# Kernel optimization log

Measured on AMD Instinct MI355X. Metric: run time of the kernel, lower is better.

The kernel has to match this reference:

```python
import jax, jax.numpy as jnp
import numpy as np

B = 128          # graphs per batch
NPG = 512        # nodes per graph
N = B * NPG      # 65536 nodes
E = 262144       # edges, avg degree 4, intra-graph only
IN_FEATS = 128
EDGE_FEATS = 32
EMB = 64
HEADS = 4
HC = EMB * HEADS  # 256
L = 3


def setup_inputs():
    ki = iter(jax.random.split(jax.random.key(0), 64))

    def nrm(shape):
        return jax.random.normal(next(ki), shape, jnp.float32)

    def lin(fan_in, shape):
        return jax.random.uniform(next(ki), shape, jnp.float32, -1.0, 1.0) / np.float32(np.sqrt(fan_in))

    x = nrm((N, IN_FEATS))
    edge_attr = nrm((E, EDGE_FEATS))
    g = jnp.arange(E) // (E // B)  # each edge stays inside its graph
    src = g * NPG + jax.random.randint(next(ki), (E,), 0, NPG)
    dst = g * NPG + jax.random.randint(next(ki), (E,), 0, NPG)
    edge_index = jnp.stack([src, dst]).astype(jnp.int32)
    batch_index = (jnp.arange(N) // NPG).astype(jnp.int32)
    d = dict(x=x, edge_attr=edge_attr, edge_index=edge_index, batch_index=batch_index)
    d['Wq1'] = lin(IN_FEATS, (IN_FEATS, HC)); d['bq1'] = lin(IN_FEATS, (HC,))
    d['Wk1'] = lin(IN_FEATS, (IN_FEATS, HC)); d['bk1'] = lin(IN_FEATS, (HC,))
    d['Wv1'] = lin(IN_FEATS, (IN_FEATS, HC)); d['bv1'] = lin(IN_FEATS, (HC,))
    d['We1'] = lin(EDGE_FEATS, (EDGE_FEATS, HC))
    d['Wskip1'] = lin(IN_FEATS, (IN_FEATS, HC)); d['bskip1'] = lin(IN_FEATS, (HC,))
    d['Wbeta1'] = lin(3 * HC, (3 * HC,))
    d['Wt1'] = lin(HC, (HC, EMB)); d['bt1'] = lin(HC, (EMB,))
    d['bng1'] = jnp.ones((EMB,), jnp.float32); d['bnb1'] = jnp.zeros((EMB,), jnp.float32)
    d['Wq'] = lin(EMB, (L, EMB, HC)); d['bq'] = lin(EMB, (L, HC))
    d['Wk'] = lin(EMB, (L, EMB, HC)); d['bk'] = lin(EMB, (L, HC))
    d['Wv'] = lin(EMB, (L, EMB, HC)); d['bv'] = lin(EMB, (L, HC))
    d['We'] = lin(EDGE_FEATS, (L, EDGE_FEATS, HC))
    d['Wskip'] = lin(EMB, (L, EMB, HC)); d['bskip'] = lin(EMB, (L, HC))
    d['Wbeta'] = lin(3 * HC, (L, 3 * HC))
    d['Wt'] = lin(HC, (L, HC, EMB)); d['bt'] = lin(HC, (L, EMB))
    d['bng'] = jnp.ones((L, EMB), jnp.float32); d['bnb'] = jnp.zeros((L, EMB), jnp.float32)
    d['pw0'] = lin(EMB, (EMB,)); d['pw2'] = lin(EMB, (EMB,))
    return d


def _tconv(x, src, dst, eattr, emask, Wq, bq, Wk, bk, Wv, bv, We, Wskip, bskip, Wbeta, n):
    # PyG TransformerConv (concat=True, beta=True, edge_dim), dropout off (eval)
    q = (x @ Wq + bq).reshape(n, HEADS, EMB)
    k = (x @ Wk + bk).reshape(n, HEADS, EMB)
    v = (x @ Wv + bv).reshape(n, HEADS, EMB)
    e = (eattr @ We).reshape(-1, HEADS, EMB)
    alpha = jnp.einsum('ehc,ehc->eh', q[dst], k[src] + e) / (EMB ** 0.5)
    alpha = jnp.where(emask[:, None], alpha, -jnp.inf)
    m = jax.ops.segment_max(alpha, dst, num_segments=n)
    m = jnp.where(jnp.isfinite(m), m, 0.0)
    p = jnp.where(emask[:, None], jnp.exp(alpha - m[dst]), 0.0)
    den = jax.ops.segment_sum(p, dst, num_segments=n)
    p = p / jnp.maximum(den, 1e-16)[dst]
    out = jax.ops.segment_sum((v[src] + e) * p[:, :, None], dst, num_segments=n).reshape(n, HC)
    xr = x @ Wskip + bskip
    beta = jax.nn.sigmoid(jnp.concatenate([out, xr, out - xr], axis=-1) @ Wbeta)[:, None]
    return beta * xr + (1.0 - beta) * out


def _bn(x, g, b):
    mu = x.mean(0)
    var = jnp.mean((x - mu) ** 2, 0)
    return (x - mu) / jnp.sqrt(var + 1e-5) * g + b


def _topk(x, src, dst, emask, w, npg, k_keep):
    # PyG TopKPooling: score = tanh(x.w / |w|), keep top ratio per graph, scale kept x by score
    n_graphs = x.shape[0] // npg
    score = jnp.tanh((x @ w) / jnp.linalg.norm(w))
    sv, idx = jax.lax.top_k(score.reshape(n_graphs, npg), k_keep)
    perm = (idx + jnp.arange(n_graphs)[:, None] * npg).reshape(-1)
    x_new = x[perm] * sv.reshape(-1)[:, None]
    new_idx = jnp.full(n_graphs * npg, -1, jnp.int32).at[perm].set(
        jnp.arange(n_graphs * k_keep, dtype=jnp.int32))
    sn, dn = new_idx[src], new_idx[dst]
    valid = emask & (sn >= 0) & (dn >= 0)
    return x_new, jnp.where(valid, sn, 0), jnp.where(valid, dn, 0), valid


def _forward(x, edge_attr, edge_index, batch_index, Wq1, bq1, Wk1, bk1, Wv1, bv1,
             We1, Wskip1, bskip1, Wbeta1, Wt1, bt1, bng1, bnb1,
             Wq, bq, Wk, bk, Wv, bv, We, Wskip, bskip, Wbeta, Wt, bt, bng, bnb,
             pw0, pw2):
    src, dst = edge_index[0], edge_index[1]
    emask = jnp.ones(src.shape, dtype=bool)
    n = x.shape[0]
    npg = n // B
    x = _tconv(x, src, dst, edge_attr, emask, Wq1, bq1, Wk1, bk1, Wv1, bv1,
               We1, Wskip1, bskip1, Wbeta1, n)
    x = _bn(jax.nn.relu(x @ Wt1 + bt1), bng1, bnb1)
    pool_w = {0: pw0, 2: pw2}
    greps = []
    for i in range(L):
        x = _tconv(x, src, dst, edge_attr, emask, Wq[i], bq[i], Wk[i], bk[i], Wv[i], bv[i],
                   We[i], Wskip[i], bskip[i], Wbeta[i], n)
        x = _bn(jax.nn.relu(x @ Wt[i] + bt[i]), bng[i], bnb[i])
        if i % 3 == 0 or i == L - 1:  # pooling at layers 0 and 2
            k_keep = npg // 2
            x, src, dst, emask = _topk(x, src, dst, emask, pool_w[i], npg, k_keep)
            npg = k_keep
            n = B * npg
            batch = jnp.arange(n) // npg  # pooled nodes stay contiguous per graph
            gmax = jax.ops.segment_max(x, batch, num_segments=B)
            gmean = jax.ops.segment_sum(x, batch, num_segments=B) / npg
            greps.append(jnp.concatenate([gmax, gmean], axis=-1))
    return greps[0] + greps[1]


def reference(x, edge_attr, edge_index, batch_index, Wq1, bq1, Wk1, bk1, Wv1, bv1,
              We1, Wskip1, bskip1, Wbeta1, Wt1, bt1, bng1, bnb1,
              Wq, bq, Wk, bk, Wv, bv, We, Wskip, bskip, Wbeta, Wt, bt, bng, bnb,
              pw0, pw2):
    return _forward(x, edge_attr, edge_index, batch_index, Wq1, bq1, Wk1, bk1, Wv1, bv1,
                    We1, Wskip1, bskip1, Wbeta1, Wt1, bt1, bng1, bnb1,
                    Wq, bq, Wk, bk, Wv, bv, We, Wskip, bskip, Wbeta, Wt, bt, bng, bnb,
                    pw0, pw2)
```

## Files before the change

kernel.cpp:

```cpp
#include <hip/hip_runtime.h>
#include <hip/hip_bf16.h>

#define NGRAPH 128
#define NTOT   65536
#define NE     262144
#define EPG    2048
#define HC     256

typedef __hip_bfloat16 bf16;

__device__ __forceinline__ float4 f4fma(float a, float4 b, float4 c){
  return make_float4(fmaf(a,b.x,c.x), fmaf(a,b.y,c.y), fmaf(a,b.z,c.z), fmaf(a,b.w,c.w));
}
__device__ __forceinline__ float4 f4add(float4 a, float4 b){
  return make_float4(a.x+b.x, a.y+b.y, a.z+b.z, a.w+b.w);
}

template<int F>
__global__ __launch_bounds__(256)
void gemm_qkvs_kernel(const float* __restrict__ X,
                      const float* __restrict__ W0, const float* __restrict__ B0,
                      const float* __restrict__ W1, const float* __restrict__ B1,
                      const float* __restrict__ W2, const float* __restrict__ B2,
                      const float* __restrict__ W3, const float* __restrict__ B3,
                      const float* __restrict__ W4, const float* __restrict__ B4,
                      float* __restrict__ Y, long ystride)
{
  const int s = blockIdx.y;
  const float* __restrict__ W = (s==0)?W0:(s==1)?W1:(s==2)?W2:(s==3)?W3:W4;
  const float* __restrict__ Bb= (s==0)?B0:(s==1)?B1:(s==2)?B2:(s==3)?B3:B4;
  float* __restrict__ Yo = Y + (long)s*ystride;

  __shared__ __align__(16) float XsT[F][36];
  const int tid  = threadIdx.x;
  const int tcol = tid & 63;
  const int trow = tid >> 6;
  const long r0 = (long)blockIdx.x * 32;
  for (int idx = tid; idx < 32*F; idx += 256){
    int r = idx / F;
    int f = idx - r*F;
    XsT[f][r] = X[(r0 + r)*F + f];
  }
  __syncthreads();
  float4 acc[8];
#pragma unroll
  for (int r = 0; r < 8; ++r) acc[r] = make_float4(0.f,0.f,0.f,0.f);
#pragma unroll 4
  for (int f = 0; f < F; ++f){
    float4 w = *(const float4*)(&W[f*HC + 4*tcol]);
    float xs[8];
    *(float4*)&xs[0] = *(const float4*)(&XsT[f][8*trow]);
    *(float4*)&xs[4] = *(const float4*)(&XsT[f][8*trow + 4]);
#pragma unroll
    for (int r = 0; r < 8; ++r) acc[r] = f4fma(xs[r], w, acc[r]);
  }
  float4 bb = *(const float4*)(&Bb[4*tcol]);
#pragma unroll
  for (int r = 0; r < 8; ++r)
    *(float4*)(&Yo[(r0 + 8*trow + r)*HC + 4*tcol]) = f4add(acc[r], bb);
}

__global__ void mcomb_kernel(const float* __restrict__ Wq,
                             const float* __restrict__ bq,
                             const float* __restrict__ We,
                             int F, float* __restrict__ M)
{
  int id = blockIdx.x*256 + threadIdx.x;
  if (id >= (F+1)*256) return;
  int g = id >> 8;
  int j = id & 255;
  float s = 0.f;
  if (j < 128){
    int h = j >> 5, f = j & 31;
    const float* row = (g < F) ? (Wq + (long)g*HC) : bq;
    const float* wr  = We + (long)f*HC + h*64;
#pragma unroll
    for (int c = 0; c < 64; ++c) s = fmaf(row[h*64 + c], wr[c], s);
  }
  M[id] = s;
}

__global__ __launch_bounds__(256)
void csr_build_kernel(const int* __restrict__ dstA, int npgLoc,
                      int* __restrict__ eids, int* __restrict__ rowptr,
                      int* __restrict__ deg)
{
  __shared__ int dloc[2048];
  __shared__ int ord[2048];
  __shared__ int cnt[512];
  __shared__ int base[512];
  const int g = blockIdx.x, tid = threadIdx.x;
  const int ebase = g*2048;
  const int nbase = g*npgLoc;
  for (int e = tid; e < 2048; e += 256){
    int d = dstA[ebase + e];
    dloc[e] = (d >= 0) ? (d - nbase) : -1;
  }
  for (int d = tid; d < npgLoc; d += 256) cnt[d] = 0;
  __syncthreads();
  for (int r = 0; r < 8; ++r){
    const int e = r*256 + tid;
    const int d = dloc[e];
    int rk = -1;
    if (d >= 0){
      rk = cnt[d];
      for (int u = r*256; u < e; ++u)
        rk += (dloc[u] == d);
    }
    ord[e] = rk;
    __syncthreads();
    if (d >= 0) atomicAdd(&cnt[d], 1);
    __syncthreads();
  }
  if (tid == 0){
    int run = 0;
    for (int d = 0; d < npgLoc; ++d){ base[d] = run; run += cnt[d]; }
  }
  __syncthreads();
  for (int e = tid; e < 2048; e += 256){
    int d = dloc[e];
    if (d >= 0) eids[ebase + base[d] + ord[e]] = ebase + e;
  }
  for (int d = tid; d < npgLoc; d += 256){
    rowptr[nbase + d] = ebase + base[d];
    deg   [nbase + d] = cnt[d];
  }
}

__global__ __launch_bounds__(256)
void attn_kernel(int nodeOff,
                 const float* q, const float* __restrict__ k,
                 const float* __restrict__ v, const float* __restrict__ skip,
                 const float* __restrict__ qwe,
                 const int* __restrict__ rowptr, const int* __restrict__ deg,
                 const int* __restrict__ eids, const int* __restrict__ srcA,
                 const float* __restrict__ EA, const float* __restrict__ We,
                 const float* __restrict__ Wb, float* xout)
{
  const int lane = threadIdx.x & 63;
  const int g16  = lane & 15;
  const int il   = blockIdx.x*4 + (threadIdx.x >> 6);
  const int i    = nodeOff + il;

  float4 q4  = *(const float4*)(&q[(long)il*HC + 4*lane]);
  float2 qw2 = *(const float2*)(&qwe[(long)il*HC + 2*lane]);

  const int p0 = rowptr[i];
  const int dg = deg[i];
  int e_l = 0, s_l = 0;
  if (lane < dg){ e_l = eids[p0 + lane]; s_l = srcA[e_l] - nodeOff; }

  float m = -__builtin_inff();
  float den = 0.f;
  float4 acc = make_float4(0.f,0.f,0.f,0.f);
  float2 wsum = make_float2(0.f,0.f);

  for (int t = 0; t < dg; ++t){
    int e, s;
    if (t < 64){ e = __shfl(e_l, t); s = __shfl(s_l, t); }
    else { e = eids[p0 + t]; s = srcA[e] - nodeOff; }
    float2 ea2 = *(const float2*)(&EA[(long)e*32 + 2*g16]);
    float4 k4  = *(const float4*)(&k[(long)s*HC + 4*lane]);
    float4 v4  = *(const float4*)(&v[(long)s*HC + 4*lane]);
    float part = q4.x*k4.x + q4.y*k4.y + q4.z*k4.z + q4.w*k4.w
               + qw2.x*ea2.x + qw2.y*ea2.y;
    part += __shfl_xor(part, 1);
    part += __shfl_xor(part, 2);
    part += __shfl_xor(part, 4);
    part += __shfl_xor(part, 8);
    float alpha = part * 0.125f;
    float nm  = fmaxf(m, alpha);
    float scl = __expf(m - nm);
    float p   = __expf(alpha - nm);
    den = den*scl + p;
    acc.x = fmaf(acc.x, scl, p*v4.x);
    acc.y = fmaf(acc.y, scl, p*v4.y);
    acc.z = fmaf(acc.z, scl, p*v4.z);
    acc.w = fmaf(acc.w, scl, p*v4.w);
    wsum.x = fmaf(wsum.x, scl, p*ea2.x);
    wsum.y = fmaf(wsum.y, scl, p*ea2.y);
    m = nm;
  }

  float4 ecorr = make_float4(0.f,0.f,0.f,0.f);
#pragma unroll
  for (int j = 0; j < 16; ++j){
    int srcl = (lane & 48) | j;
    float wx = __shfl(wsum.x, srcl);
    float wy = __shfl(wsum.y, srcl);
    float4 w0 = *(const float4*)(&We[(2*j)*HC + 4*lane]);
    float4 w1 = *(const float4*)(&We[(2*j+1)*HC + 4*lane]);
    ecorr = f4fma(wx, w0, ecorr);
    ecorr = f4fma(wy, w1, ecorr);
  }
  float inv = 1.f / fmaxf(den, 1e-16f);
  float4 o = make_float4((acc.x+ecorr.x)*inv, (acc.y+ecorr.y)*inv,
                         (acc.z+ecorr.z)*inv, (acc.w+ecorr.w)*inv);

  float4 xr  = *(const float4*)(&skip[(long)il*HC + 4*lane]);
  float4 wb1 = *(const float4*)(&Wb[4*lane]);
  float4 wb2 = *(const float4*)(&Wb[HC + 4*lane]);
  float4 wb3 = *(const float4*)(&Wb[2*HC + 4*lane]);
  float tp = o.x*wb1.x + o.y*wb1.y + o.z*wb1.z + o.w*wb1.w
           + xr.x*wb2.x + xr.y*wb2.y + xr.z*wb2.z + xr.w*wb2.w
           + (o.x-xr.x)*wb3.x + (o.y-xr.y)*wb3.y
           + (o.z-xr.z)*wb3.z + (o.w-xr.w)*wb3.w;
  tp += __shfl_xor(tp, 1);
  tp += __shfl_xor(tp, 2);
  tp += __shfl_xor(tp, 4);
  tp += __shfl_xor(tp, 8);
  tp += __shfl_xor(tp, 16);
  tp += __shfl_xor(tp, 32);
  float beta = 1.f / (1.f + __expf(-tp));
  float4 xo = make_float4(beta*xr.x + (1.f-beta)*o.x,
                          beta*xr.y + (1.f-beta)*o.y,
                          beta*xr.z + (1.f-beta)*o.z,
                          beta*xr.w + (1.f-beta)*o.w);
  *(float4*)(&xout[(long)il*HC + 4*lane]) = xo;
}

__global__ __launch_bounds__(256)
void gemm_wt_kernel(const float* __restrict__ Xa, const float* __restrict__ Wt,
                    const float* __restrict__ bt, float* __restrict__ y,
                    float* __restrict__ psum, float* __restrict__ psq, int blkBase)
{
  __shared__ __align__(16) float XsT[64][132];
  const int tid  = threadIdx.x;
  const int tcol = tid & 15;
  const int trow = tid >> 4;
  const long r0 = (long)blockIdx.x * 128;
  float4 acc[8];
#pragma unroll
  for (int r = 0; r < 8; ++r) acc[r] = make_float4(0.f,0.f,0.f,0.f);
  for (int kc = 0; kc < 4; ++kc){
    for (int idx = tid; idx < 128*64; idx += 256){
      int r = idx >> 6;
      int f = idx & 63;
      XsT[f][r] = Xa[(r0 + r)*HC + kc*64 + f];
    }
    __syncthreads();
#pragma unroll 4
    for (int f = 0; f < 64; ++f){
      float4 w = *(const float4*)(&Wt[(kc*64 + f)*64 + 4*tcol]);
      float xs[8];
      *(float4*)&xs[0] = *(const float4*)(&XsT[f][8*trow]);
      *(float4*)&xs[4] = *(const float4*)(&XsT[f][8*trow + 4]);
#pragma unroll
      for (int r = 0; r < 8; ++r) acc[r] = f4fma(xs[r], w, acc[r]);
    }
    __syncthreads();
  }
  float4 bb = *(const float4*)(&bt[4*tcol]);
  float4 ls = make_float4(0.f,0.f,0.f,0.f);
  float4 lq = make_float4(0.f,0.f,0.f,0.f);
#pragma unroll
  for (int r = 0; r < 8; ++r){
    float4 o = f4add(acc[r], bb);
    o.x = fmaxf(o.x, 0.f); o.y = fmaxf(o.y, 0.f);
    o.z = fmaxf(o.z, 0.f); o.w = fmaxf(o.w, 0.f);
    *(float4*)(&y[(r0 + 8*trow + r)*64 + 4*tcol]) = o;
    ls.x += o.x; ls.y += o.y; ls.z += o.z; ls.w += o.w;
    lq.x += o.x*o.x; lq.y += o.y*o.y; lq.z += o.z*o.z; lq.w += o.w*o.w;
  }
  float* s1 = &XsT[0][0];
  float* s2 = s1 + 1024;
  *(float4*)&s1[trow*64 + 4*tcol] = ls;
  *(float4*)&s2[trow*64 + 4*tcol] = lq;
  __syncthreads();
  if (tid < 64){
    float a = 0.f, b = 0.f;
#pragma unroll
    for (int t = 0; t < 16; ++t){
      a += s1[t*64 + tid];
      b += s2[t*64 + tid];
    }
    psum[(long)(blkBase + blockIdx.x)*64 + tid] = a;
    psq [(long)(blkBase + blockIdx.x)*64 + tid] = b;
  }
}

__global__ void bn_finalize_kernel(const float* __restrict__ psum,
                                   const float* __restrict__ psq,
                                   int nblocks, float n_f, float* musd)
{
  __shared__ float s1[4][64], s2[4][64];
  const int col = threadIdx.x & 63;
  const int part = threadIdx.x >> 6;
  float a = 0.f, b = 0.f;
  for (int j = part; j < nblocks; j += 4){
    a += psum[(long)j*64 + col];
    b += psq [(long)j*64 + col];
  }
  s1[part][col] = a; s2[part][col] = b;
  __syncthreads();
  if (threadIdx.x < 64){
    int c = threadIdx.x;
    float sa = s1[0][c] + s1[1][c] + s1[2][c] + s1[3][c];
    float sb = s2[0][c] + s2[1][c] + s2[2][c] + s2[3][c];
    float mu = sa / n_f;
    float var = sb / n_f - mu*mu;
    musd[c] = mu;
    musd[64 + c] = rsqrtf(var + 1e-5f);
  }
}

__global__ void bn_apply_kernel(float* y, const float* __restrict__ musd,
                                const float* __restrict__ g,
                                const float* __restrict__ b, long total)
{
  long i4 = ((long)blockIdx.x * 256 + threadIdx.x) * 4;
  if (i4 >= total) return;
  int c0 = (int)(i4 & 63);
  float4 yv = *(float4*)&y[i4];
  yv.x = (yv.x - musd[c0+0]) * musd[64+c0+0] * g[c0+0] + b[c0+0];
  yv.y = (yv.y - musd[c0+1]) * musd[64+c0+1] * g[c0+1] + b[c0+1];
  yv.z = (yv.z - musd[c0+2]) * musd[64+c0+2] * g[c0+2] + b[c0+2];
  yv.w = (yv.w - musd[c0+3]) * musd[64+c0+3] * g[c0+3] + b[c0+3];
  *(float4*)&y[i4] = yv;
}

__global__ __launch_bounds__(256)
void topk_kernel(const float* __restrict__ x, const float* __restrict__ pw,
                 float* __restrict__ x2, int* __restrict__ newidx,
                 int npg, int kkeep)
{
  __shared__ float sc[512];
  __shared__ float wS[64];
  const int g = blockIdx.x, tid = threadIdx.x;
  if (tid < 64) wS[tid] = pw[tid];
  __syncthreads();
  float nrm = 0.f;
#pragma unroll
  for (int c = 0; c < 64; ++c) nrm += wS[c]*wS[c];
  nrm = sqrtf(nrm);
  for (int il = tid; il < npg; il += 256){
    const float* xr = x + (long)(g*npg + il)*64;
    float d = 0.f;
    for (int c = 0; c < 64; ++c) d = fmaf(xr[c], wS[c], d);
    sc[il] = tanhf(d / nrm);
  }
  __syncthreads();
  for (int il = tid; il < npg; il += 256){
    float si = sc[il];
    int r = 0;
    for (int j = 0; j < npg; ++j){
      float sj = sc[j];
      r += (sj > si) || (sj == si && j < il);
    }
    int gi = g*npg + il;
    if (r < kkeep){
      int npos = g*kkeep + r;
      newidx[gi] = npos;
      const float4* xr4 = (const float4*)(x + (long)gi*64);
      float4* xo4 = (float4*)(x2 + (long)npos*64);
#pragma unroll
      for (int c4 = 0; c4 < 16; ++c4){
        float4 xv = xr4[c4];
        xo4[c4] = make_float4(xv.x*si, xv.y*si, xv.z*si, xv.w*si);
      }
    } else {
      newidx[gi] = -1;
    }
  }
}

__global__ void remap_kernel(const int* __restrict__ src0, const int* __restrict__ dst0,
                             const int* __restrict__ newidx,
                             int* __restrict__ src2, int* __restrict__ dst2)
{
  int e = blockIdx.x * 256 + threadIdx.x;
  int ns = newidx[src0[e]];
  int nd = newidx[dst0[e]];
  bool ok = (ns >= 0) && (nd >= 0);
  src2[e] = ok ? ns : 0;
  dst2[e] = ok ? nd : -1;
}

__global__ void gpool_kernel(const float* __restrict__ x2, int kkeep,
                             float* grep0, float* out, int mode)
{
  const int g = blockIdx.x, c = threadIdx.x;
  float mx = -__builtin_inff(), s = 0.f;
  for (int j = 0; j < kkeep; ++j){
    float vv = x2[((long)g*kkeep + j)*64 + c];
    mx = fmaxf(mx, vv);
    s += vv;
  }
  float mean = s / (float)kkeep;
  if (mode == 0){
    grep0[g*128 + c] = mx;
    grep0[g*128 + 64 + c] = mean;
  } else {
    out[g*128 + c]      = grep0[g*128 + c] + mx;
    out[g*128 + 64 + c] = grep0[g*128 + 64 + c] + mean;
  }
}

extern "C" void kernel_launch(void* const* d_in, const int* in_sizes, int n_in,
                              void* d_out, int out_size, void* d_ws, size_t ws_size,
                              hipStream_t stream)
{
  const float* x_in = (const float*)d_in[0];
  const float* EA   = (const float*)d_in[1];
  const int*   eidx = (const int*)d_in[2];
  const int*   src0 = eidx;
  const int*   dst0 = eidx + NE;

  const float* Wq1    = (const float*)d_in[4];
  const float* bq1    = (const float*)d_in[5];
  const float* Wk1    = (const float*)d_in[6];
  const float* bk1    = (const float*)d_in[7];
  const float* Wv1    = (const float*)d_in[8];
  const float* bv1    = (const float*)d_in[9];
  const float* We1    = (const float*)d_in[10];
  const float* Wskip1 = (const float*)d_in[11];
  const float* bskip1 = (const float*)d_in[12];
  const float* Wbeta1 = (const float*)d_in[13];
  const float* Wt1    = (const float*)d_in[14];
  const float* bt1    = (const float*)d_in[15];
  const float* bng1   = (const float*)d_in[16];
  const float* bnb1   = (const float*)d_in[17];
  const float* WqL    = (const float*)d_in[18];
  const float* bqL    = (const float*)d_in[19];
  const float* WkL    = (const float*)d_in[20];
  const float* bkL    = (const float*)d_in[21];
  const float* WvL    = (const float*)d_in[22];
  const float* bvL    = (const float*)d_in[23];
  const float* WeL    = (const float*)d_in[24];
  const float* WskipL = (const float*)d_in[25];
  const float* bskipL = (const float*)d_in[26];
  const float* WbetaL = (const float*)d_in[27];
  const float* WtL    = (const float*)d_in[28];
  const float* btL    = (const float*)d_in[29];
  const float* bngL   = (const float*)d_in[30];
  const float* bnbL   = (const float*)d_in[31];
  const float* pw0    = (const float*)d_in[32];
  const float* pw2    = (const float*)d_in[33];

  const size_t FIXED = 33554432ull;
  int chunks = 1;
  while (chunks < 32 && 5ull*(67108864ull/chunks) + FIXED > ws_size)
    chunks <<= 1;
  const int gpc = NGRAPH / chunks;
  const size_t C = 67108864ull / chunks;
  const long CF = (long)(C / 4);

  char* wsb = (char*)d_ws;
  float* qb   = (float*)(wsb);
  float* kb   = (float*)(wsb + C);
  float* vb   = (float*)(wsb + 2*C);
  float* sk   = (float*)(wsb + 3*C);
  float* qweb = (float*)(wsb + 4*C);
  char* p = wsb + 5*C;
  auto alloc = [&](size_t bytes){ char* r = p; p += (bytes + 255) & ~255ull; return r; };
  float* y      = (float*)alloc(16777216ull);
  float* x2     = (float*)alloc(8388608ull);
  float* ps     = (float*)alloc(131072ull);
  float* pq     = (float*)alloc(131072ull);
  float* musd   = (float*)alloc(4096ull);
  float* grep0  = (float*)alloc(65536ull);
  float* Mbuf   = (float*)alloc(132608ull);
  int* newidx   = (int*)alloc(262144ull);
  int* src2     = (int*)alloc(1048576ull);
  int* dst2     = (int*)alloc(1048576ull);
  int* eidsA    = (int*)alloc(1048576ull);
  int* rowptrA  = (int*)alloc(262144ull);
  int* degA     = (int*)alloc(262144ull);
  int* eidsB    = (int*)alloc(1048576ull);
  int* rowptrB  = (int*)alloc(131072ull);
  int* degB     = (int*)alloc(131072ull);

  csr_build_kernel<<<NGRAPH, 256, 0, stream>>>(dst0, 512, eidsA, rowptrA, degA);

  {
    const int npg = 512, n = NTOT;
    mcomb_kernel<<<129, 256, 0, stream>>>(Wq1, bq1, We1, 128, Mbuf);
    for (int c = 0; c < chunks; ++c){
      const int nOff = c * gpc * npg;
      const int nc   = gpc * npg;
      const float* Xc = x_in + (long)nOff * 128;
      dim3 grid(nc/32, 5);
      gemm_qkvs_kernel<128><<<grid, 256, 0, stream>>>(
          Xc, Wq1, bq1, Wk1, bk1, Wv1, bv1, Wskip1, bskip1,
          Mbuf, Mbuf + 128*256, qb, CF);
      attn_kernel<<<nc/4, 256, 0, stream>>>(nOff, qb, kb, vb, sk, qweb,
          rowptrA, degA, eidsA, src0, EA, We1, Wbeta1, qb);
      gemm_wt_kernel<<<nc/128, 256, 0, stream>>>(qb, Wt1, bt1,
          y + (long)nOff*64, ps, pq, nOff/128);
    }
    bn_finalize_kernel<<<1, 256, 0, stream>>>(ps, pq, n/128, (float)n, musd);
    bn_apply_kernel<<<n/16, 256, 0, stream>>>(y, musd, bng1, bnb1, (long)n*64);
  }

  for (int i = 0; i < 3; ++i){
    const int n   = (i == 0) ? NTOT : NTOT/2;
    const int npg = (i == 0) ? 512 : 256;
    const float* xin = (i == 0) ? y : ((i == 1) ? x2 : y);
    const int* rp = (i == 0) ? rowptrA : rowptrB;
    const int* dgp= (i == 0) ? degA    : degB;
    const int* ei = (i == 0) ? eidsA   : eidsB;
    const int* sA = (i == 0) ? src0    : src2;
    const float* Wq_ = WqL + (long)i*64*256;  const float* bq_ = bqL + i*256;
    const float* Wk_ = WkL + (long)i*64*256;  const float* bk_ = bkL + i*256;
    const float* Wv_ = WvL + (long)i*64*256;  const float* bv_ = bvL + i*256;
    const float* Ws_ = WskipL + (long)i*64*256; const float* bs_ = bskipL + i*256;
    const float* We_ = WeL + (long)i*32*256;
    const float* Wb_ = WbetaL + i*768;
    const float* Wt_ = WtL + (long)i*256*64;  const float* bt_ = btL + i*64;
    const float* g_  = bngL + i*64;           const float* b_  = bnbL + i*64;

    mcomb_kernel<<<65, 256, 0, stream>>>(Wq_, bq_, We_, 64, Mbuf);
    for (int c = 0; c < chunks; ++c){
      const int nOff = c * gpc * npg;
      const int nc   = gpc * npg;
      const float* Xc = xin + (long)nOff * 64;
      dim3 grid(nc/32, 5);
      gemm_qkvs_kernel<64><<<grid, 256, 0, stream>>>(
          Xc, Wq_, bq_, Wk_, bk_, Wv_, bv_, Ws_, bs_,
          Mbuf, Mbuf + 64*256, qb, CF);
      attn_kernel<<<nc/4, 256, 0, stream>>>(nOff, qb, kb, vb, sk, qweb,
          rp, dgp, ei, sA, EA, We_, Wb_, qb);
      gemm_wt_kernel<<<nc/128, 256, 0, stream>>>(qb, Wt_, bt_,
          y + (long)nOff*64, ps, pq, nOff/128);
    }
    bn_finalize_kernel<<<1, 256, 0, stream>>>(ps, pq, n/128, (float)n, musd);
    bn_apply_kernel<<<n/16, 256, 0, stream>>>(y, musd, g_, b_, (long)n*64);

    if (i == 0){
      topk_kernel<<<NGRAPH, 256, 0, stream>>>(y, pw0, x2, newidx, 512, 256);
      remap_kernel<<<NE/256, 256, 0, stream>>>(src0, dst0, newidx, src2, dst2);
      csr_build_kernel<<<NGRAPH, 256, 0, stream>>>(dst2, 256, eidsB, rowptrB, degB);
      gpool_kernel<<<NGRAPH, 64, 0, stream>>>(x2, 256, grep0, (float*)d_out, 0);
    } else if (i == 2){
      topk_kernel<<<NGRAPH, 256, 0, stream>>>(y, pw2, x2, newidx, 256, 128);
      gpool_kernel<<<NGRAPH, 64, 0, stream>>>(x2, 128, grep0, (float*)d_out, 1);
    }
  }

  (void)in_sizes; (void)n_in; (void)out_size; (void)ws_size;
}
```

Before: 1.576 ms.

## Fuse batchnorm apply into consumers and prefetch next edge in attention

Removes the standalone bn_apply kernel and instead applies the normalization lazily when the next gemm_qkvs loads its input tile, or inside topk when scoring and copying pooled rows. This saves a full read-modify-write pass over the activations after each layer, at the cost of extra per-element arithmetic in the loaders and strided scalar loads in topk. The attention loop is also software-pipelined so that the k, v and edge-attribute loads for the next edge are issued before the current edge is processed, which hides gather latency but uses more registers. A __syncthreads is added before shared memory is reused for the BN partial sums.

Result: no change. 1.607 ms (+2.0%).

```diff
diff --git a/kernel.cpp b/kernel.cpp
--- a/kernel.cpp
+++ b/kernel.cpp
@@ -24,6 +24,8 @@
                       const float* __restrict__ W2, const float* __restrict__ B2,
                       const float* __restrict__ W3, const float* __restrict__ B3,
                       const float* __restrict__ W4, const float* __restrict__ B4,
+                      const float* __restrict__ musd, const float* __restrict__ bng,
+                      const float* __restrict__ bnb,
                       float* __restrict__ Y, long ystride)
 {
   const int s = blockIdx.y;
@@ -39,7 +41,9 @@
   for (int idx = tid; idx < 32*F; idx += 256){
     int r = idx / F;
     int f = idx - r*F;
-    XsT[f][r] = X[(r0 + r)*F + f];
+    float xv = X[(r0 + r)*F + f];
+    if (musd) xv = (xv - musd[f]) * musd[64+f] * bng[f] + bnb[f];
+    XsT[f][r] = xv;
   }
   __syncthreads();
   float4 acc[8];
@@ -155,15 +159,29 @@
   float4 acc = make_float4(0.f,0.f,0.f,0.f);
   float2 wsum = make_float2(0.f,0.f);
 
+  float2 eaC = make_float2(0.f,0.f);
+  float4 kC  = make_float4(0.f,0.f,0.f,0.f);
+  float4 vC  = make_float4(0.f,0.f,0.f,0.f);
+  if (dg > 0){
+    int e = __shfl(e_l, 0), s = __shfl(s_l, 0);
+    eaC = *(const float2*)(&EA[(long)e*32 + 2*g16]);
+    kC  = *(const float4*)(&k[(long)s*HC + 4*lane]);
+    vC  = *(const float4*)(&v[(long)s*HC + 4*lane]);
+  }
+
   for (int t = 0; t < dg; ++t){
-    int e, s;
-    if (t < 64){ e = __shfl(e_l, t); s = __shfl(s_l, t); }
-    else { e = eids[p0 + t]; s = srcA[e] - nodeOff; }
-    float2 ea2 = *(const float2*)(&EA[(long)e*32 + 2*g16]);
-    float4 k4  = *(const float4*)(&k[(long)s*HC + 4*lane]);
-    float4 v4  = *(const float4*)(&v[(long)s*HC + 4*lane]);
-    float part = q4.x*k4.x + q4.y*k4.y + q4.z*k4.z + q4.w*k4.w
-               + qw2.x*ea2.x + qw2.y*ea2.y;
+    float2 eaN; float4 kN, vN;
+    const bool more = (t+1 < dg);
+    if (more){
+      int e, s;
+      if (t+1 < 64){ e = __shfl(e_l, t+1); s = __shfl(s_l, t+1); }
+      else { e = eids[p0 + t + 1]; s = srcA[e] - nodeOff; }
+      eaN = *(const float2*)(&EA[(long)e*32 + 2*g16]);
+      kN  = *(const float4*)(&k[(long)s*HC + 4*lane]);
+      vN  = *(const float4*)(&v[(long)s*HC + 4*lane]);
+    }
+    float part = q4.x*kC.x + q4.y*kC.y + q4.z*kC.z + q4.w*kC.w
+               + qw2.x*eaC.x + qw2.y*eaC.y;
     part += __shfl_xor(part, 1);
     part += __shfl_xor(part, 2);
     part += __shfl_xor(part, 4);
@@ -173,13 +191,14 @@
     float scl = __expf(m - nm);
     float p   = __expf(alpha - nm);
     den = den*scl + p;
-    acc.x = fmaf(acc.x, scl, p*v4.x);
-    acc.y = fmaf(acc.y, scl, p*v4.y);
-    acc.z = fmaf(acc.z, scl, p*v4.z);
-    acc.w = fmaf(acc.w, scl, p*v4.w);
-    wsum.x = fmaf(wsum.x, scl, p*ea2.x);
-    wsum.y = fmaf(wsum.y, scl, p*ea2.y);
+    acc.x = fmaf(acc.x, scl, p*vC.x);
+    acc.y = fmaf(acc.y, scl, p*vC.y);
+    acc.z = fmaf(acc.z, scl, p*vC.z);
+    acc.w = fmaf(acc.w, scl, p*vC.w);
+    wsum.x = fmaf(wsum.x, scl, p*eaC.x);
+    wsum.y = fmaf(wsum.y, scl, p*eaC.y);
     m = nm;
+    if (more){ eaC = eaN; kC = kN; vC = vN; }
   }
 
   float4 ecorr = make_float4(0.f,0.f,0.f,0.f);
@@ -264,6 +283,7 @@
   }
   float* s1 = &XsT[0][0];
   float* s2 = s1 + 1024;
+  __syncthreads();
   *(float4*)&s1[trow*64 + 4*tcol] = ls;
   *(float4*)&s2[trow*64 + 4*tcol] = lq;
   __syncthreads();
@@ -304,30 +324,21 @@
   }
 }
 
-__global__ void bn_apply_kernel(float* y, const float* __restrict__ musd,
-                                const float* __restrict__ g,
-                                const float* __restrict__ b, long total)
-{
-  long i4 = ((long)blockIdx.x * 256 + threadIdx.x) * 4;
-  if (i4 >= total) return;
-  int c0 = (int)(i4 & 63);
-  float4 yv = *(float4*)&y[i4];
-  yv.x = (yv.x - musd[c0+0]) * musd[64+c0+0] * g[c0+0] + b[c0+0];
-  yv.y = (yv.y - musd[c0+1]) * musd[64+c0+1] * g[c0+1] + b[c0+1];
-  yv.z = (yv.z - musd[c0+2]) * musd[64+c0+2] * g[c0+2] + b[c0+2];
-  yv.w = (yv.w - musd[c0+3]) * musd[64+c0+3] * g[c0+3] + b[c0+3];
-  *(float4*)&y[i4] = yv;
-}
-
 __global__ __launch_bounds__(256)
 void topk_kernel(const float* __restrict__ x, const float* __restrict__ pw,
+                 const float* __restrict__ musd, const float* __restrict__ g_,
+                 const float* __restrict__ b_,
                  float* __restrict__ x2, int* __restrict__ newidx,
                  int npg, int kkeep)
 {
   __shared__ float sc[512];
-  __shared__ float wS[64];
+  __shared__ float wS[64], muS[64], sdS[64], gS[64], bS[64];
   const int g = blockIdx.x, tid = threadIdx.x;
-  if (tid < 64) wS[tid] = pw[tid];
+  if (tid < 64){
+    wS[tid] = pw[tid];
+    muS[tid] = musd[tid]; sdS[tid] = musd[64+tid];
+    gS[tid] = g_[tid]; bS[tid] = b_[tid];
+  }
   __syncthreads();
   float nrm = 0.f;
 #pragma unroll
@@ -336,7 +347,10 @@
   for (int il = tid; il < npg; il += 256){
     const float* xr = x + (long)(g*npg + il)*64;
     float d = 0.f;
-    for (int c = 0; c < 64; ++c) d = fmaf(xr[c], wS[c], d);
+    for (int c = 0; c < 64; ++c){
+      float bnv = (xr[c] - muS[c]) * sdS[c] * gS[c] + bS[c];
+      d = fmaf(bnv, wS[c], d);
+    }
     sc[il] = tanhf(d / nrm);
   }
   __syncthreads();
@@ -351,12 +365,12 @@
     if (r < kkeep){
       int npos = g*kkeep + r;
       newidx[gi] = npos;
-      const float4* xr4 = (const float4*)(x + (long)gi*64);
-      float4* xo4 = (float4*)(x2 + (long)npos*64);
-#pragma unroll
-      for (int c4 = 0; c4 < 16; ++c4){
-        float4 xv = xr4[c4];
-        xo4[c4] = make_float4(xv.x*si, xv.y*si, xv.z*si, xv.w*si);
+      const float* xr = x + (long)gi*64;
+      float* xo = x2 + (long)npos*64;
+#pragma unroll 4
+      for (int c = 0; c < 64; ++c){
+        float bnv = (xr[c] - muS[c]) * sdS[c] * gS[c] + bS[c];
+        xo[c] = bnv * si;
       }
     } else {
       newidx[gi] = -1;
@@ -482,20 +496,22 @@
       dim3 grid(nc/32, 5);
       gemm_qkvs_kernel<128><<<grid, 256, 0, stream>>>(
           Xc, Wq1, bq1, Wk1, bk1, Wv1, bv1, Wskip1, bskip1,
-          Mbuf, Mbuf + 128*256, qb, CF);
+          Mbuf, Mbuf + 128*256, nullptr, nullptr, nullptr, qb, CF);
       attn_kernel<<<nc/4, 256, 0, stream>>>(nOff, qb, kb, vb, sk, qweb,
           rowptrA, degA, eidsA, src0, EA, We1, Wbeta1, qb);
       gemm_wt_kernel<<<nc/128, 256, 0, stream>>>(qb, Wt1, bt1,
           y + (long)nOff*64, ps, pq, nOff/128);
     }
     bn_finalize_kernel<<<1, 256, 0, stream>>>(ps, pq, n/128, (float)n, musd);
-    bn_apply_kernel<<<n/16, 256, 0, stream>>>(y, musd, bng1, bnb1, (long)n*64);
   }
 
   for (int i = 0; i < 3; ++i){
     const int n   = (i == 0) ? NTOT : NTOT/2;
     const int npg = (i == 0) ? 512 : 256;
     const float* xin = (i == 0) ? y : ((i == 1) ? x2 : y);
+    const float* stg_g = (i == 0) ? bng1 : ((i == 2) ? bngL + 1*64 : nullptr);
+    const float* stg_b = (i == 0) ? bnb1 : ((i == 2) ? bnbL + 1*64 : nullptr);
+    const float* stg_m = (i == 1) ? nullptr : musd;
     const int* rp = (i == 0) ? rowptrA : rowptrB;
     const int* dgp= (i == 0) ? degA    : degB;
     const int* ei = (i == 0) ? eidsA   : eidsB;
@@ -517,22 +533,23 @@
       dim3 grid(nc/32, 5);
       gemm_qkvs_kernel<64><<<grid, 256, 0, stream>>>(
           Xc, Wq_, bq_, Wk_, bk_, Wv_, bv_, Ws_, bs_,
-          Mbuf, Mbuf + 64*256, qb, CF);
+          Mbuf, Mbuf + 64*256, stg_m, stg_g, stg_b, qb, CF);
       attn_kernel<<<nc/4, 256, 0, stream>>>(nOff, qb, kb, vb, sk, qweb,
           rp, dgp, ei, sA, EA, We_, Wb_, qb);
       gemm_wt_kernel<<<nc/128, 256, 0, stream>>>(qb, Wt_, bt_,
           y + (long)nOff*64, ps, pq, nOff/128);
     }
     bn_finalize_kernel<<<1, 256, 0, stream>>>(ps, pq, n/128, (float)n, musd);
-    bn_apply_kernel<<<n/16, 256, 0, stream>>>(y, musd, g_, b_, (long)n*64);
 
     if (i == 0){
-      topk_kernel<<<NGRAPH, 256, 0, stream>>>(y, pw0, x2, newidx, 512, 256);
+      topk_kernel<<<NGRAPH, 256, 0, stream>>>(y, pw0, musd, g_, b_,
+                                              x2, newidx, 512, 256);
       remap_kernel<<<NE/256, 256, 0, stream>>>(src0, dst0, newidx, src2, dst2);
       csr_build_kernel<<<NGRAPH, 256, 0, stream>>>(dst2, 256, eidsB, rowptrB, degB);
       gpool_kernel<<<NGRAPH, 64, 0, stream>>>(x2, 256, grep0, (float*)d_out, 0);
     } else if (i == 2){
-      topk_kernel<<<NGRAPH, 256, 0, stream>>>(y, pw2, x2, newidx, 256, 128);
+      topk_kernel<<<NGRAPH, 256, 0, stream>>>(y, pw2, musd, g_, b_,
+                                              x2, newidx, 256, 128);
       gpool_kernel<<<NGRAPH, 64, 0, stream>>>(x2, 128, grep0, (float*)d_out, 1);
     }
   }
```
